# Kernel optimization log

Hardware: AMD Instinct MI355X
Metric: run time of the kernel (lower is better)

Reference implementation:

```python
import jax, jax.numpy as jnp
import numpy as np

EMBED_DIM = 768
NUM_HEADS = 12
HEAD_DIM = EMBED_DIM // NUM_HEADS  # 64
NUM_LEVELS = 2
Q_INDEX = (0, 6, 12)  # head-axis split per level
K_INDEX = (0, 6, 12)
V_INDEX = (0, 6, 12)


def setup_inputs() -> dict:
    key = jax.random.key(0)
    ks = jax.random.split(key, 12)
    std = 0.02
    d = {
        'inp0': jax.random.normal(ks[0], (8, 2048, 768), jnp.float32),
        'inp1': jax.random.normal(ks[1], (8, 1024, 1536), jnp.float32),
        'attn_mask': jax.random.normal(ks[2], (8, HEAD_DIM), jnp.float32),
        'Wq0': jax.random.normal(ks[3], (768, 768), jnp.float32) * std,
        'bq0': jnp.zeros((768,), jnp.float32),
        'Wk0': jax.random.normal(ks[4], (768, 768), jnp.float32) * std,
        'bk0': jnp.zeros((768,), jnp.float32),
        'Wv0': jax.random.normal(ks[5], (768, 768), jnp.float32) * std,
        'bv0': jnp.zeros((768,), jnp.float32),
        'Wq1': jax.random.normal(ks[6], (1536, 768), jnp.float32) * std,
        'bq1': jnp.zeros((768,), jnp.float32),
        'Wk1': jax.random.normal(ks[7], (1536, 768), jnp.float32) * std,
        'bk1': jnp.zeros((768,), jnp.float32),
        'Wv1': jax.random.normal(ks[8], (1536, 768), jnp.float32) * std,
        'bv1': jnp.zeros((768,), jnp.float32),
        'Wo': jax.random.normal(ks[9], (2 * 768, 768), jnp.float32) * std,
        'bo': jnp.zeros((768,), jnp.float32),
    }
    return d


def _split_heads(x):
    b, n, _ = x.shape
    return x.reshape(b, n, NUM_HEADS, HEAD_DIM).transpose(0, 2, 1, 3)  # b h n d


def _level_attention(level, inp, Wq, bq, Wk, bk, Wv, bv, attn_mask):
    q = _split_heads(inp @ Wq + bq)[:, Q_INDEX[level]:Q_INDEX[level + 1]]
    k = _split_heads(inp @ Wk + bk)[:, K_INDEX[level]:K_INDEX[level + 1]]
    v = _split_heads(inp @ Wv + bv)[:, V_INDEX[level]:V_INDEX[level + 1]]
    q = q * (HEAD_DIM ** -0.5)
    q = q + attn_mask[:, None, None, :]  # broadcast mask over heads & positions
    scores = jnp.einsum('bhnd,bhmd->bhnm', q, k)
    attn = jax.nn.softmax(scores, axis=-1)
    return jnp.einsum('bhnm,bhmd->bhnd', attn, v)  # b h n d


def reference(inp0, inp1, attn_mask, Wq0, bq0, Wk0, bk0, Wv0, bv0,
              Wq1, bq1, Wk1, bk1, Wv1, bv1, Wo, bo):
    levels = [
        (inp0, Wq0, bq0, Wk0, bk0, Wv0, bv0),
        (inp1, Wq1, bq1, Wk1, bk1, Wv1, bv1),
    ]
    outputs = [_level_attention(l, *args, attn_mask) for l, args in enumerate(levels)]
    n_max = max(o.shape[2] for o in outputs)
    merged, masks = [], []
    for o in outputs:
        b, h, n, dd = o.shape
        x = o.transpose(0, 2, 1, 3).reshape(b, n, h * dd)  # b n (h d)
        x = jnp.pad(x, ((0, 0), (0, n_max - n), (0, EMBED_DIM - h * dd)))
        merged.append(x)
        masks.append(jnp.pad(jnp.ones((n,), jnp.float32), (0, n_max - n)))
    x = jnp.concatenate(merged, axis=-1)  # [b, n_max, NUM_LEVELS*EMBED_DIM]
    output_mask = jnp.stack(masks)  # [NUM_LEVELS, n_max]
    output = x @ Wo + bo
    return (output, output_mask)
```

## Files before the change

kernel.cpp:

```cpp
#include <hip/hip_runtime.h>
#include <cmath>

typedef __bf16 bf16x8 __attribute__((ext_vector_type(8)));
typedef float floatx4 __attribute__((ext_vector_type(4)));

typedef __attribute__((address_space(1))) const void* as1_cvp;
typedef __attribute__((address_space(3))) void* as3_vp;

__device__ __forceinline__ void stage16(const void* g, void* l) {
    __builtin_amdgcn_global_load_lds((as1_cvp)g, (as3_vp)l, 16, 0, 0);
}

__global__ void prep_all(
    const float* __restrict__ inp0, const float* __restrict__ inp1,
    const float* __restrict__ Wq0, const float* __restrict__ Wk0, const float* __restrict__ Wv0,
    const float* __restrict__ Wq1, const float* __restrict__ Wk1, const float* __restrict__ Wv1,
    const float* __restrict__ Wo,
    __bf16* __restrict__ Ab0, __bf16* __restrict__ Ab1,
    __bf16* __restrict__ WT0, __bf16* __restrict__ WT1, __bf16* __restrict__ WoT)
{
    __shared__ __bf16 tile[64][72];
    const int bx = blockIdx.x;
    const int tid = threadIdx.x;

    if (bx < 12288) {
        const float* in  = (bx < 6144) ? inp0 : inp1;
        __bf16*      out = (bx < 6144) ? Ab0  : Ab1;
        int t = (bx < 6144 ? bx : bx - 6144) * 256 + tid;
        floatx4 f0 = *(const floatx4*)&in[(size_t)t * 8];
        floatx4 f1 = *(const floatx4*)&in[(size_t)t * 8 + 4];
        bf16x8 o;
#pragma unroll
        for (int j = 0; j < 4; j++) { o[j] = (__bf16)f0[j]; o[4 + j] = (__bf16)f1[j]; }
        *(bf16x8*)&out[(size_t)t * 8] = o;
        return;
    }

    int lane = tid & 63, tr = tid >> 6;

    if (bx < 12936) {
        int seg1 = (bx >= 12504);
        int idx = seg1 ? bx - 12504 : bx - 12288;
        int nkb = seg1 ? 24 : 12;
        int Kd  = seg1 ? 1536 : 768;
        int off = seg1 ? 384 : 0;
        int k0 = (idx % nkb) * 64, c0 = (idx / nkb) * 64;
        int proj = c0 / 384;
        const float* src = seg1 ? ((proj == 0) ? Wq1 : (proj == 1) ? Wk1 : Wv1)
                                : ((proj == 0) ? Wq0 : (proj == 1) ? Wk0 : Wv0);
        __bf16* WT = seg1 ? WT1 : WT0;
        int col = off + (c0 % 384) + lane;
#pragma unroll
        for (int i = 0; i < 16; i++) {
            int r = i * 4 + tr;
            tile[lane][r] = (__bf16)src[(size_t)(k0 + r) * 768 + col];
        }
        __syncthreads();
#pragma unroll
        for (int i = 0; i < 16; i++) {
            int cl = i * 4 + tr;
            WT[(size_t)(c0 + cl) * Kd + k0 + lane] = tile[cl][lane];
        }
        return;
    }

    {
        int idx = bx - 12936;
        int k0 = (idx % 12) * 64, c0 = (idx / 12) * 64;
        int col = c0 + lane;
#pragma unroll
        for (int i = 0; i < 16; i++) {
            int k = k0 + i * 4 + tr;
            int srow = k + (k >= 384 ? 384 : 0);
            tile[lane][i * 4 + tr] = (__bf16)Wo[(size_t)srow * 768 + col];
        }
        __syncthreads();
#pragma unroll
        for (int i = 0; i < 16; i++) {
            int cl = i * 4 + tr;
            WoT[(size_t)(c0 + cl) * 768 + k0 + lane] = tile[cl][lane];
        }
        return;
    }
}

__global__ __launch_bounds__(256, 2) void qkv_all(
    const __bf16* __restrict__ Ab0, const __bf16* __restrict__ Ab1,
    const __bf16* __restrict__ WT0, const __bf16* __restrict__ WT1,
    const float* __restrict__ bq0, const float* __restrict__ bk0, const float* __restrict__ bv0,
    const float* __restrict__ bq1, const float* __restrict__ bk1, const float* __restrict__ bv1,
    const float* __restrict__ mask,
    __bf16* __restrict__ Q0, __bf16* __restrict__ K0, __bf16* __restrict__ V0T,
    __bf16* __restrict__ Q1, __bf16* __restrict__ K1, __bf16* __restrict__ V1T)
{
    __shared__ __bf16 As[2][128 * 64];
    __shared__ __bf16 Bs[2][128 * 64];
    const int p = blockIdx.x;
    int bx;
    if (p < 1152) bx = (p & 7) * 144 + (p >> 3);
    else { int q = p - 1152; bx = 1152 + (q & 7) * 72 + (q >> 3); }
    const int seg = (bx >= 1152);
    const int idx = seg ? bx - 1152 : bx;
    const int Kd  = seg ? 1536 : 768;
    const int Nl  = seg ? 1024 : 2048;
    const int nlsh = seg ? 10 : 11;
    const int off = seg ? 384 : 0;
    const __bf16* A  = seg ? Ab1 : Ab0;
    const __bf16* BT = seg ? WT1 : WT0;
    const float* bq = seg ? bq1 : bq0;
    const float* bk = seg ? bk1 : bk0;
    const float* bv = seg ? bv1 : bv0;
    __bf16* Qo  = seg ? Q1 : Q0;
    __bf16* Ko  = seg ? K1 : K0;
    __bf16* VTo = seg ? V1T : V0T;

    const int tid = threadIdx.x;
    const int lane = tid & 63;
    const int wave = tid >> 6;
    const int lr = lane & 15, lg = lane >> 4;
    const int col0 = (idx % 9) * 128, row0 = (idx / 9) * 128;
    const int qr = (wave >> 1) * 64, qc = (wave & 1) * 64;
    floatx4 acc[4][4] = {};

    const int schunk = ((lane & 7) ^ (lane >> 3)) * 8;
    const __bf16* ga0 = A  + (size_t)(row0 + wave * 32 + (lane >> 3)) * Kd + schunk;
    const __bf16* gb0 = BT + (size_t)(col0 + wave * 32 + (lane >> 3)) * Kd + schunk;

    const int nsteps = Kd >> 6;

#pragma unroll
    for (int i = 0; i < 4; i++) {
        stage16(ga0 + (size_t)i * 8 * Kd, &As[0][(wave * 32 + i * 8) * 64]);
        stage16(gb0 + (size_t)i * 8 * Kd, &Bs[0][(wave * 32 + i * 8) * 64]);
    }
    __syncthreads();

    int cur = 0;
    for (int t = 0; t < nsteps; ++t) {
        if (t + 1 < nsteps) {
            int k0 = (t + 1) << 6;
#pragma unroll
            for (int i = 0; i < 4; i++) {
                stage16(ga0 + (size_t)i * 8 * Kd + k0, &As[cur ^ 1][(wave * 32 + i * 8) * 64]);
                stage16(gb0 + (size_t)i * 8 * Kd + k0, &Bs[cur ^ 1][(wave * 32 + i * 8) * 64]);
            }
        }
#pragma unroll
        for (int ch = 0; ch < 2; ch++) {
            bf16x8 af[4], bfr[4];
#pragma unroll
            for (int mt = 0; mt < 4; mt++)
                af[mt] = *(const bf16x8*)&As[cur][(qr + mt * 16 + lr) * 64
                                                 + (((ch * 4 + lg) ^ (lr & 7)) * 8)];
#pragma unroll
            for (int nt = 0; nt < 4; nt++)
                bfr[nt] = *(const bf16x8*)&Bs[cur][(qc + nt * 16 + lr) * 64
                                                  + (((ch * 4 + lg) ^ (lr & 7)) * 8)];
#pragma unroll
            for (int mt = 0; mt < 4; mt++)
#pragma unroll
                for (int nt = 0; nt < 4; nt++)
                    acc[mt][nt] = __builtin_amdgcn_mfma_f32_16x16x32_bf16(af[mt], bfr[nt], acc[mt][nt], 0, 0, 0);
        }
        if (t + 1 < nsteps) {
            __syncthreads();
            cur ^= 1;
        }
    }

    const float S_Q = 0.125f * 1.44269504088896f;
    const float S_M = 1.44269504088896f;
#pragma unroll
    for (int nt = 0; nt < 4; nt++) {
        int C = col0 + qc + nt * 16 + lr;
        int proj = C / 384;
        int rem = C - proj * 384;
        int h = rem >> 6, d = C & 63;
        float bias = (proj == 0) ? bq[off + rem]
                   : (proj == 1) ? bk[off + rem]
                                 : bv[off + rem];
#pragma unroll
        for (int mt = 0; mt < 4; mt++) {
#pragma unroll
            for (int r = 0; r < 4; r++) {
                int R = row0 + qr + mt * 16 + lg * 4 + r;
                int b = R >> nlsh;
                int n = R & (Nl - 1);
                size_t hb = (size_t)(b * 6 + h);
                float v = acc[mt][nt][r] + bias;
                if (proj == 0) {
                    v = fmaf(v, S_Q, S_M * mask[(b << 6) + d]);
                    Qo[(hb * Nl + n) * 64 + d] = (__bf16)v;
                } else if (proj == 1) {
                    Ko[(hb * Nl + n) * 64 + d] = (__bf16)v;
                } else {
                    VTo[(hb * 64 + d) * (size_t)Nl + n] = (__bf16)v;
                }
            }
        }
    }
}

__global__ __launch_bounds__(256, 4) void attn_all(
    const __bf16* __restrict__ Q0, const __bf16* __restrict__ K0, const __bf16* __restrict__ V0T,
    const __bf16* __restrict__ Q1, const __bf16* __restrict__ K1, const __bf16* __restrict__ V1T,
    __bf16* __restrict__ X, float* __restrict__ om)
{
    __shared__ __bf16 Ks[64 * 72];
    __shared__ __bf16 Vs[64 * 72];
    __shared__ __bf16 Ps[4][32 * 72];
    const int p = blockIdx.x;
    int bx;
    if (p < 768) bx = (p & 7) * 96 + (p >> 3);
    else if (p < 1152) { int q = p - 768; bx = 768 + (q & 7) * 48 + (q >> 3); }
    else bx = p;
    const int tid = threadIdx.x;

    if (bx >= 1152) {
        int t = (bx - 1152) * 256 + tid;
        int r = t / 48;
        int c = (t - r * 48) * 8;
        int b = r >> 10, n = 1024 + (r & 1023);
        floatx4 z = {0.f, 0.f, 0.f, 0.f};
        *(floatx4*)&X[(size_t)(b * 2048 + n) * 768 + 384 + c] = z;
        if (t < 4096)
            om[t] = (t < 2048) ? 1.0f : (((t - 2048) < 1024) ? 1.0f : 0.0f);
        return;
    }

    const int seg = (bx >= 768);
    const int idx = seg ? bx - 768 : bx;
    const int Nl = seg ? 1024 : 2048;
    const int qb = seg ? (idx & 7) : (idx & 15);
    const int rest = seg ? (idx >> 3) : (idx >> 4);
    const int h = rest % 6, b = rest / 6;
    const int xoff = seg ? 384 : 0;
    const __bf16* Q  = seg ? Q1 : Q0;
    const __bf16* K  = seg ? K1 : K0;
    const __bf16* VT = seg ? V1T : V0T;

    const int wave = tid >> 6, lane = tid & 63;
    const int lr = lane & 15, lg = lane >> 4;
    const size_t head = (size_t)(b * 6 + h) * Nl * 64;
    const int q0 = qb * 128 + wave * 16;

    bf16x8 qf[2][2];
#pragma unroll
    for (int s = 0; s < 2; s++)
#pragma unroll
        for (int ch = 0; ch < 2; ch++)
            qf[s][ch] = *(const bf16x8*)&Q[head + (size_t)(q0 + s * 64 + lr) * 64 + ch * 32 + lg * 8];

    bf16x8 onesv;
#pragma unroll
    for (int j = 0; j < 8; j++) onesv[j] = (__bf16)1.0f;

    const int rr = tid >> 2, cc = (tid & 3) * 16;
    const __bf16* Kg = K + head;
    const __bf16* Vg = VT + head;

    bf16x8 kr0, kr1, vr0, vr1;
    {
        size_t kb = (size_t)rr * 64 + cc;
        kr0 = *(const bf16x8*)&Kg[kb];
        kr1 = *(const bf16x8*)&Kg[kb + 8];
        size_t vb = (size_t)rr * Nl + cc;
        vr0 = *(const bf16x8*)&Vg[vb];
        vr1 = *(const bf16x8*)&Vg[vb + 8];
    }

    floatx4 o_acc[2][4] = {};
    floatx4 l_acc[2] = {};

    for (int n0 = 0; n0 < Nl; n0 += 64) {
        __syncthreads();
        *(bf16x8*)&Ks[rr * 72 + cc]     = kr0;
        *(bf16x8*)&Ks[rr * 72 + cc + 8] = kr1;
        *(bf16x8*)&Vs[rr * 72 + cc]     = vr0;
        *(bf16x8*)&Vs[rr * 72 + cc + 8] = vr1;
        __syncthreads();

        if (n0 + 64 < Nl) {
            size_t kb = (size_t)(n0 + 64 + rr) * 64 + cc;
            kr0 = *(const bf16x8*)&Kg[kb];
            kr1 = *(const bf16x8*)&Kg[kb + 8];
            size_t vb = (size_t)rr * Nl + n0 + 64 + cc;
            vr0 = *(const bf16x8*)&Vg[vb];
            vr1 = *(const bf16x8*)&Vg[vb + 8];
        }

        floatx4 sv[2][4] = {};
        __builtin_amdgcn_s_setprio(1);
#pragma unroll
        for (int ch = 0; ch < 2; ch++) {
#pragma unroll
            for (int nt = 0; nt < 4; nt++) {
                bf16x8 kb8 = *(const bf16x8*)&Ks[(nt * 16 + lr) * 72 + ch * 32 + lg * 8];
                sv[0][nt] = __builtin_amdgcn_mfma_f32_16x16x32_bf16(qf[0][ch], kb8, sv[0][nt], 0, 0, 0);
                sv[1][nt] = __builtin_amdgcn_mfma_f32_16x16x32_bf16(qf[1][ch], kb8, sv[1][nt], 0, 0, 0);
            }
        }
        __builtin_amdgcn_s_setprio(0);

#pragma unroll
        for (int s = 0; s < 2; s++)
#pragma unroll
            for (int nt = 0; nt < 4; nt++)
#pragma unroll
                for (int r = 0; r < 4; r++) {
                    float p2 = __builtin_amdgcn_exp2f(sv[s][nt][r]);
                    Ps[wave][(s * 16 + lg * 4 + r) * 72 + nt * 16 + lr] = (__bf16)p2;
                }
        asm volatile("s_waitcnt lgkmcnt(0)" ::: "memory");

        __builtin_amdgcn_s_setprio(1);
#pragma unroll
        for (int ch = 0; ch < 2; ch++) {
            bf16x8 pa0 = *(const bf16x8*)&Ps[wave][lr * 72 + ch * 32 + lg * 8];
            bf16x8 pa1 = *(const bf16x8*)&Ps[wave][(16 + lr) * 72 + ch * 32 + lg * 8];
#pragma unroll
            for (int dt = 0; dt < 4; dt++) {
                bf16x8 vb8 = *(const bf16x8*)&Vs[(dt * 16 + lr) * 72 + ch * 32 + lg * 8];
                o_acc[0][dt] = __builtin_amdgcn_mfma_f32_16x16x32_bf16(pa0, vb8, o_acc[0][dt], 0, 0, 0);
                o_acc[1][dt] = __builtin_amdgcn_mfma_f32_16x16x32_bf16(pa1, vb8, o_acc[1][dt], 0, 0, 0);
            }
            l_acc[0] = __builtin_amdgcn_mfma_f32_16x16x32_bf16(pa0, onesv, l_acc[0], 0, 0, 0);
            l_acc[1] = __builtin_amdgcn_mfma_f32_16x16x32_bf16(pa1, onesv, l_acc[1], 0, 0, 0);
        }
        __builtin_amdgcn_s_setprio(0);
    }

#pragma unroll
    for (int s = 0; s < 2; s++)
#pragma unroll
        for (int dt = 0; dt < 4; dt++)
#pragma unroll
            for (int r = 0; r < 4; r++) {
                int n = q0 + s * 64 + lg * 4 + r;
                float o = o_acc[s][dt][r] / l_acc[s][r];
                X[(size_t)(b * 2048 + n) * 768 + xoff + h * 64 + dt * 16 + lr] = (__bf16)o;
            }
}

__global__ __launch_bounds__(256, 2) void out_gemm(
    const __bf16* __restrict__ A, const __bf16* __restrict__ BT,
    const float* __restrict__ bo, float* __restrict__ out)
{
    __shared__ __bf16 As[2][128 * 64];
    __shared__ __bf16 Bs[2][128 * 64];
    const int tid = threadIdx.x;
    const int lane = tid & 63;
    const int wave = tid >> 6;
    const int lr = lane & 15, lg = lane >> 4;
    const int p = blockIdx.x;
    const int bx = (p & 7) * 96 + (p >> 3);
    const int col0 = (bx % 6) * 128, row0 = (bx / 6) * 128;
    const int qr = (wave >> 1) * 64, qc = (wave & 1) * 64;
    const int Kd = 768;
    floatx4 acc[4][4] = {};

    const int schunk = ((lane & 7) ^ (lane >> 3)) * 8;
    const __bf16* ga0 = A  + (size_t)(row0 + wave * 32 + (lane >> 3)) * Kd + schunk;
    const __bf16* gb0 = BT + (size_t)(col0 + wave * 32 + (lane >> 3)) * Kd + schunk;
    const int nsteps = Kd >> 6;

#pragma unroll
    for (int i = 0; i < 4; i++) {
        stage16(ga0 + (size_t)i * 8 * Kd, &As[0][(wave * 32 + i * 8) * 64]);
        stage16(gb0 + (size_t)i * 8 * Kd, &Bs[0][(wave * 32 + i * 8) * 64]);
    }
    __syncthreads();

    int cur = 0;
    for (int t = 0; t < nsteps; ++t) {
        if (t + 1 < nsteps) {
            int k0 = (t + 1) << 6;
#pragma unroll
            for (int i = 0; i < 4; i++) {
                stage16(ga0 + (size_t)i * 8 * Kd + k0, &As[cur ^ 1][(wave * 32 + i * 8) * 64]);
                stage16(gb0 + (size_t)i * 8 * Kd + k0, &Bs[cur ^ 1][(wave * 32 + i * 8) * 64]);
            }
        }
#pragma unroll
        for (int ch = 0; ch < 2; ch++) {
            bf16x8 af[4], bfr[4];
#pragma unroll
            for (int mt = 0; mt < 4; mt++)
                af[mt] = *(const bf16x8*)&As[cur][(qr + mt * 16 + lr) * 64
                                                 + (((ch * 4 + lg) ^ (lr & 7)) * 8)];
#pragma unroll
            for (int nt = 0; nt < 4; nt++)
                bfr[nt] = *(const bf16x8*)&Bs[cur][(qc + nt * 16 + lr) * 64
                                                  + (((ch * 4 + lg) ^ (lr & 7)) * 8)];
#pragma unroll
            for (int mt = 0; mt < 4; mt++)
#pragma unroll
                for (int nt = 0; nt < 4; nt++)
                    acc[mt][nt] = __builtin_amdgcn_mfma_f32_16x16x32_bf16(af[mt], bfr[nt], acc[mt][nt], 0, 0, 0);
        }
        if (t + 1 < nsteps) {
            __syncthreads();
            cur ^= 1;
        }
    }

#pragma unroll
    for (int nt = 0; nt < 4; nt++) {
        int C = col0 + qc + nt * 16 + lr;
        float bias = bo[C];
#pragma unroll
        for (int mt = 0; mt < 4; mt++) {
#pragma unroll
            for (int r = 0; r < 4; r++) {
                int R = row0 + qr + mt * 16 + lg * 4 + r;
                out[(size_t)R * 768 + C] = acc[mt][nt][r] + bias;
            }
        }
    }
}

extern "C" void kernel_launch(void* const* d_in, const int* in_sizes, int n_in,
                              void* d_out, int out_size, void* d_ws, size_t ws_size,
                              hipStream_t stream)
{
    const float* inp0  = (const float*)d_in[0];
    const float* inp1  = (const float*)d_in[1];
    const float* amask = (const float*)d_in[2];
    const float* Wq0 = (const float*)d_in[3];
    const float* bq0 = (const float*)d_in[4];
    const float* Wk0 = (const float*)d_in[5];
    const float* bk0 = (const float*)d_in[6];
    const float* Wv0 = (const float*)d_in[7];
    const float* bv0 = (const float*)d_in[8];
    const float* Wq1 = (const float*)d_in[9];
    const float* bq1 = (const float*)d_in[10];
    const float* Wk1 = (const float*)d_in[11];
    const float* bk1 = (const float*)d_in[12];
    const float* Wv1 = (const float*)d_in[13];
    const float* bv1 = (const float*)d_in[14];
    const float* Wo  = (const float*)d_in[15];
    const float* bo  = (const float*)d_in[16];

    char* ws = (char*)d_ws;
    __bf16* WT0 = (__bf16*)(ws + 0);
    __bf16* WT1 = (__bf16*)(ws + 1769472);
    __bf16* WoT = (__bf16*)(ws + 5308416);
    __bf16* Ab0 = (__bf16*)(ws + 6488064);
    __bf16* X   = Ab0;
    __bf16* Ab1 = (__bf16*)(ws + 31653888);
    __bf16* Q0  = (__bf16*)(ws + 56819712);
    __bf16* K0  = (__bf16*)(ws + 69402624);
    __bf16* V0T = (__bf16*)(ws + 81985536);
    __bf16* Q1  = (__bf16*)(ws + 94568448);
    __bf16* K1  = (__bf16*)(ws + 100859904);
    __bf16* V1T = (__bf16*)(ws + 107151360);
    float* outp = (float*)d_out;

    hipLaunchKernelGGL(prep_all, dim3(13080), dim3(256), 0, stream,
                       inp0, inp1, Wq0, Wk0, Wv0, Wq1, Wk1, Wv1, Wo,
                       Ab0, Ab1, WT0, WT1, WoT);
    hipLaunchKernelGGL(qkv_all, dim3(1728), dim3(256), 0, stream,
                       Ab0, Ab1, WT0, WT1,
                       bq0, bk0, bv0, bq1, bk1, bv1, amask,
                       Q0, K0, V0T, Q1, K1, V1T);
    hipLaunchKernelGGL(attn_all, dim3(2688), dim3(256), 0, stream,
                       Q0, K0, V0T, Q1, K1, V1T, X, outp + 12582912);
    hipLaunchKernelGGL(out_gemm, dim3(768), dim3(256), 0, stream,
                       X, WoT, bo, outp);
}
```

Measured before the change: 431.8 us.

## Use partial vmcnt waits and raw barriers in GEMM loops, reorder tiles

Both GEMM mainloops now issue the next tile's async LDS loads and then wait only until the current tile's loads are done (vmcnt(8)), rather than draining everything through __syncthreads. Raw s_barrier calls, one before and one after compute, replace the old synchronisation. MFMA sections run at raised wave priority via s_setprio. The QKV kernel also launches the longer K=1536 level-1 tiles first to balance the tail. The hand-written waitcnt depends on the compiler not reordering or adding other vector memory ops, which is a correctness risk.

Measured after the change: 403.2 us. -6.6%, faster.

```diff
diff --git a/kernel.cpp b/kernel.cpp
--- a/kernel.cpp
+++ b/kernel.cpp
@@ -97,8 +97,8 @@
     __shared__ __bf16 Bs[2][128 * 64];
     const int p = blockIdx.x;
     int bx;
-    if (p < 1152) bx = (p & 7) * 144 + (p >> 3);
-    else { int q = p - 1152; bx = 1152 + (q & 7) * 72 + (q >> 3); }
+    if (p < 576) { bx = 1152 + (p & 7) * 72 + (p >> 3); }
+    else { int q = p - 576; bx = (q & 7) * 144 + (q >> 3); }
     const int seg = (bx >= 1152);
     const int idx = seg ? bx - 1152 : bx;
     const int Kd  = seg ? 1536 : 768;
@@ -125,26 +125,31 @@
     const int schunk = ((lane & 7) ^ (lane >> 3)) * 8;
     const __bf16* ga0 = A  + (size_t)(row0 + wave * 32 + (lane >> 3)) * Kd + schunk;
     const __bf16* gb0 = BT + (size_t)(col0 + wave * 32 + (lane >> 3)) * Kd + schunk;
-
     const int nsteps = Kd >> 6;
 
 #pragma unroll
     for (int i = 0; i < 4; i++) {
-        stage16(ga0 + (size_t)i * 8 * Kd, &As[0][(wave * 32 + i * 8) * 64]);
-        stage16(gb0 + (size_t)i * 8 * Kd, &Bs[0][(wave * 32 + i * 8) * 64]);
-    }
-    __syncthreads();
-
-    int cur = 0;
+        stage16(ga0 + (size_t)(i * 8) * Kd, &As[0][(wave * 32 + i * 8) * 64]);
+        stage16(gb0 + (size_t)(i * 8) * Kd, &Bs[0][(wave * 32 + i * 8) * 64]);
+    }
+
     for (int t = 0; t < nsteps; ++t) {
+        const int cur = t & 1;
         if (t + 1 < nsteps) {
-            int k0 = (t + 1) << 6;
+            const int k0 = (t + 1) << 6;
+            const int nb = cur ^ 1;
 #pragma unroll
             for (int i = 0; i < 4; i++) {
-                stage16(ga0 + (size_t)i * 8 * Kd + k0, &As[cur ^ 1][(wave * 32 + i * 8) * 64]);
-                stage16(gb0 + (size_t)i * 8 * Kd + k0, &Bs[cur ^ 1][(wave * 32 + i * 8) * 64]);
-            }
-        }
+                stage16(ga0 + (size_t)(i * 8) * Kd + k0, &As[nb][(wave * 32 + i * 8) * 64]);
+                stage16(gb0 + (size_t)(i * 8) * Kd + k0, &Bs[nb][(wave * 32 + i * 8) * 64]);
+            }
+            asm volatile("s_waitcnt vmcnt(8)" ::: "memory");
+        } else {
+            asm volatile("s_waitcnt vmcnt(0)" ::: "memory");
+        }
+        __builtin_amdgcn_s_barrier();
+
+        __builtin_amdgcn_s_setprio(1);
 #pragma unroll
         for (int ch = 0; ch < 2; ch++) {
             bf16x8 af[4], bfr[4];
@@ -162,10 +167,8 @@
                 for (int nt = 0; nt < 4; nt++)
                     acc[mt][nt] = __builtin_amdgcn_mfma_f32_16x16x32_bf16(af[mt], bfr[nt], acc[mt][nt], 0, 0, 0);
         }
-        if (t + 1 < nsteps) {
-            __syncthreads();
-            cur ^= 1;
-        }
+        __builtin_amdgcn_s_setprio(0);
+        __builtin_amdgcn_s_barrier();
     }
 
     const float S_Q = 0.125f * 1.44269504088896f;
@@ -366,21 +369,27 @@
 
 #pragma unroll
     for (int i = 0; i < 4; i++) {
-        stage16(ga0 + (size_t)i * 8 * Kd, &As[0][(wave * 32 + i * 8) * 64]);
-        stage16(gb0 + (size_t)i * 8 * Kd, &Bs[0][(wave * 32 + i * 8) * 64]);
-    }
-    __syncthreads();
-
-    int cur = 0;
+        stage16(ga0 + (size_t)(i * 8) * Kd, &As[0][(wave * 32 + i * 8) * 64]);
+        stage16(gb0 + (size_t)(i * 8) * Kd, &Bs[0][(wave * 32 + i * 8) * 64]);
+    }
+
     for (int t = 0; t < nsteps; ++t) {
+        const int cur = t & 1;
         if (t + 1 < nsteps) {
-            int k0 = (t + 1) << 6;
+            const int k0 = (t + 1) << 6;
+            const int nb = cur ^ 1;
 #pragma unroll
             for (int i = 0; i < 4; i++) {
-                stage16(ga0 + (size_t)i * 8 * Kd + k0, &As[cur ^ 1][(wave * 32 + i * 8) * 64]);
-                stage16(gb0 + (size_t)i * 8 * Kd + k0, &Bs[cur ^ 1][(wave * 32 + i * 8) * 64]);
-            }
-        }
+                stage16(ga0 + (size_t)(i * 8) * Kd + k0, &As[nb][(wave * 32 + i * 8) * 64]);
+                stage16(gb0 + (size_t)(i * 8) * Kd + k0, &Bs[nb][(wave * 32 + i * 8) * 64]);
+            }
+            asm volatile("s_waitcnt vmcnt(8)" ::: "memory");
+        } else {
+            asm volatile("s_waitcnt vmcnt(0)" ::: "memory");
+        }
+        __builtin_amdgcn_s_barrier();
+
+        __builtin_amdgcn_s_setprio(1);
 #pragma unroll
         for (int ch = 0; ch < 2; ch++) {
             bf16x8 af[4], bfr[4];
@@ -398,10 +407,8 @@
                 for (int nt = 0; nt < 4; nt++)
                     acc[mt][nt] = __builtin_amdgcn_mfma_f32_16x16x32_bf16(af[mt], bfr[nt], acc[mt][nt], 0, 0, 0);
         }
-        if (t + 1 < nsteps) {
-            __syncthreads();
-            cur ^= 1;
-        }
+        __builtin_amdgcn_s_setprio(0);
+        __builtin_amdgcn_s_barrier();
     }
 
 #pragma unroll
```
